# Kernel optimization log

Hardware: AMD Instinct MI355X
Metric: run time of the kernel (lower is better)

## Reference

```python
import jax, jax.numpy as jnp
import numpy as np

B, L, V, E, H, T = 32, 512, 100000, 300, 256, 4  # H = hidden_dim//2 per direction


def setup_inputs() -> dict:
    key = jax.random.key(0)
    ks = jax.random.split(key, 16)
    word_ids = jax.random.randint(ks[0], (B, L), 0, V, dtype=jnp.int32)
    mask = jnp.ones((B, L), dtype=jnp.int32)
    label_ids = jax.random.randint(ks[1], (B, L), 0, T, dtype=jnp.int32)
    emb = jax.random.uniform(ks[2], (V, E), minval=-0.25, maxval=0.25, dtype=jnp.float32)
    emb = emb.at[0].set(0.0)  # padding_idx=0
    w = lambda k, s: jax.random.normal(k, s, dtype=jnp.float32) * 0.05
    return {
        "word_ids": word_ids, "mask": mask, "label_ids": label_ids,
        "emb": emb,
        "Wih_f": w(ks[3], (4 * H, E)), "Whh_f": w(ks[4], (4 * H, H)), "b_f": jnp.zeros((4 * H,), jnp.float32),
        "Wih_b": w(ks[5], (4 * H, E)), "Whh_b": w(ks[6], (4 * H, H)), "b_b": jnp.zeros((4 * H,), jnp.float32),
        "W_out": w(ks[7], (T, 2 * H)), "b_out": jnp.zeros((T,), jnp.float32),
        "transitions": w(ks[8], (T, T)), "start_trans": w(ks[9], (T,)), "end_trans": w(ks[10], (T,)),
    }


def _lstm_dir(x, Wih, Whh, b):
    # x: [B, L, E] -> hs: [B, L, H]; PyTorch gate order i, f, g, o
    xg = jnp.einsum('ble,ge->blg', x, Wih) + b  # [B, L, 4H]
    h0 = jnp.zeros((x.shape[0], Whh.shape[1]), x.dtype)

    def step(carry, g):
        h, c = carry
        gates = g + h @ Whh.T
        i, f, gg, o = jnp.split(gates, 4, axis=-1)
        c = jax.nn.sigmoid(f) * c + jax.nn.sigmoid(i) * jnp.tanh(gg)
        h = jax.nn.sigmoid(o) * jnp.tanh(c)
        return (h, c), h

    _, hs = jax.lax.scan(step, (h0, h0), jnp.swapaxes(xg, 0, 1))
    return jnp.swapaxes(hs, 0, 1)


def _emissions(word_ids, emb, Wih_f, Whh_f, b_f, Wih_b, Whh_b, b_b, W_out, b_out):
    x = emb[word_ids]                                   # [B, L, E]
    h_fwd = _lstm_dir(x, Wih_f, Whh_f, b_f)
    h_bwd = _lstm_dir(x[:, ::-1], Wih_b, Whh_b, b_b)[:, ::-1]
    h = jnp.concatenate([h_fwd, h_bwd], axis=-1)        # [B, L, 2H]
    return h @ W_out.T + b_out                          # [B, L, T]


def _viterbi_decode(emissions, mask, transitions, start_trans, end_trans):
    m = mask.astype(bool)
    score0 = start_trans + emissions[:, 0]              # [B, T]

    def step(score, inp):
        emit_t, mask_t = inp                            # [B,T], [B]
        cand = score[:, :, None] + transitions[None] + emit_t[:, None, :]  # [B, T_from, T_to]
        idx = jnp.argmax(cand, axis=1).astype(jnp.int32)
        new = jnp.max(cand, axis=1)
        return jnp.where(mask_t[:, None], new, score), idx

    score, history = jax.lax.scan(
        step, score0,
        (jnp.swapaxes(emissions[:, 1:], 0, 1), jnp.swapaxes(m[:, 1:], 0, 1)))
    score = score + end_trans
    last_tag = jnp.argmax(score, axis=-1).astype(jnp.int32)  # [B]

    def back(tag, inp):
        idx_t, mask_t = inp
        prev = jnp.take_along_axis(idx_t, tag[:, None], axis=1)[:, 0]
        tag = jnp.where(mask_t, prev, tag)
        return tag, tag

    _, tags_rev = jax.lax.scan(back, last_tag,
                               (history, jnp.swapaxes(m[:, 1:], 0, 1)), reverse=True)
    tags = jnp.concatenate([jnp.swapaxes(tags_rev, 0, 1), last_tag[:, None]], axis=1)  # [B, L]
    return tags * mask.astype(jnp.int32)  # zero out padding like torch y_pred init


def reference(word_ids, mask, label_ids, emb, Wih_f, Whh_f, b_f, Wih_b, Whh_b, b_b,
              W_out, b_out, transitions, start_trans, end_trans):
    emissions = _emissions(word_ids, emb, Wih_f, Whh_f, b_f, Wih_b, Whh_b, b_b, W_out, b_out)
    return _viterbi_decode(emissions, mask, transitions, start_trans, end_trans)
```

## Files before the change

kernel.cpp:

```cpp
#include <hip/hip_runtime.h>
#include <math.h>

#define B_   32
#define L_   512
#define E_   300
#define H_   256
#define T_   4
#define NTOK 16384
#define XGLD 2048
#define SENT 2.0f

typedef float f32x4 __attribute__((ext_vector_type(4)));
typedef float f32x2 __attribute__((ext_vector_type(2)));

__device__ __forceinline__ float fsigmoid_(float x) { return 1.0f / (1.0f + __expf(-x)); }
__device__ __forceinline__ float ftanh_(float x) {
  return 1.0f - 2.0f / (__expf(2.0f * x) + 1.0f);
}

__device__ __forceinline__ void llc_store_f32(float* p, float v) {
  asm volatile("global_store_dword %0, %1, off sc0 sc1" :: "v"(p), "v"(v) : "memory");
}
__device__ __forceinline__ void llc_store_f32x4(float* p, f32x4 v) {
  asm volatile("global_store_dwordx4 %0, %1, off sc0 sc1" :: "v"(p), "v"(v) : "memory");
}
__device__ __forceinline__ f32x4 llc_load_f32x4(const float* p) {
  f32x4 r;
  asm volatile("global_load_dwordx4 %0, %1, off sc0 sc1" : "=&v"(r) : "v"(p) : "memory");
  return r;
}

#define XBM 128
#define XBN 128
#define XBK 20
__global__ __launch_bounds__(256) void xproj_kernel(
    const int*   __restrict__ wid,
    const float* __restrict__ emb,
    const float* __restrict__ wih_f,
    const float* __restrict__ wih_b,
    const float* __restrict__ b_f,
    const float* __restrict__ b_b,
    float* __restrict__ xg,
    float*       h_all,
    int          n4)
{
  __shared__ float Ast[XBK][XBM];
  __shared__ float Bst[XBK][XBN];
  __shared__ int   wid_s[XBM];

  const int tid = threadIdx.x;
  const int m0 = blockIdx.y * XBM;
  const int n0 = blockIdx.x * XBN;
  const int d  = n0 >> 10;
  const float* wih  = d ? wih_b : wih_f;
  const float* bias = d ? b_b  : b_f;
  const int g0 = n0 & 1023;

  if (tid < XBM) wid_s[tid] = wid[m0 + tid];
  __syncthreads();

  const int srow = tid & 127;
  const int half = tid >> 7;
  const float* sbase = half ? (wih + (size_t)(g0 + srow) * E_)
                            : (emb + (size_t)wid_s[srow] * E_);
  float* sdst = half ? &Bst[0][0] : &Ast[0][0];

  f32x4 pre[5];
#pragma unroll
  for (int qd = 0; qd < 5; ++qd) pre[qd] = *(const f32x4*)(sbase + qd * 4);

  const int tx = tid & 15, ty = tid >> 4;
  float acc[8][8] = {};

  for (int k0 = 0; k0 < 300; k0 += XBK) {
#pragma unroll
    for (int qd = 0; qd < 5; ++qd)
#pragma unroll
      for (int e = 0; e < 4; ++e)
        sdst[(qd * 4 + e) * XBM + srow] = pre[qd][e];
    if (k0 + XBK < 300) {
      const float* p = sbase + k0 + XBK;
#pragma unroll
      for (int qd = 0; qd < 5; ++qd) pre[qd] = *(const f32x4*)(p + qd * 4);
    }
    __syncthreads();

#pragma unroll
    for (int k = 0; k < XBK; ++k) {
      float av[8], bv[8];
      *(f32x4*)&av[0] = *(const f32x4*)&Ast[k][ty * 8];
      *(f32x4*)&av[4] = *(const f32x4*)&Ast[k][ty * 8 + 4];
      *(f32x4*)&bv[0] = *(const f32x4*)&Bst[k][tx * 8];
      *(f32x4*)&bv[4] = *(const f32x4*)&Bst[k][tx * 8 + 4];
#pragma unroll
      for (int i = 0; i < 8; ++i)
#pragma unroll
        for (int j = 0; j < 8; ++j)
          acc[i][j] += av[i] * bv[j];
    }
    __syncthreads();
  }

#pragma unroll
  for (int i = 0; i < 8; ++i) {
    const int r = m0 + ty * 8 + i;
    float* op = xg + (size_t)r * XGLD + n0 + tx * 8;
#pragma unroll
    for (int j = 0; j < 8; ++j)
      op[j] = acc[i][j] + bias[g0 + tx * 8 + j];
  }

  {
    const int blin = blockIdx.y * 16 + blockIdx.x;
    f32x4 sv = {SENT, SENT, SENT, SENT};
    for (int i = blin * 256 + tid; i < n4; i += 2048 * 256)
      llc_store_f32x4(h_all + (size_t)i * 4, sv);
  }
}

__global__ __launch_bounds__(512, 2) void lstm_kernel(
    const float* __restrict__ xg,
    const float* __restrict__ whh_f,
    const float* __restrict__ whh_b,
    float*       h_all)
{
  const int bid = blockIdx.x;
  const int d   = bid >> 7;
  const int q   = (bid >> 4) & 7;
  const int sl  = bid & 15;
  const int tid = threadIdx.x;
  const int kp  = tid >> 6;
  const int lane = tid & 63;
  const int bl_loc = lane >> 5;
  const int rg  = lane & 31;
  const float* __restrict__ whh = d ? whh_b : whh_f;

  __shared__ float h_lds[4 * 260];
  __shared__ float part_lds[2 * 8 * 2 * 72];

  f32x4 wreg[2][8];
#pragma unroll
  for (int r = 0; r < 2; ++r) {
    const int row_l = rg * 2 + r;
    const int u  = row_l >> 2;
    const int gt = row_l & 3;
    const int grow = gt * 256 + sl * 16 + u;
    const float* rp = whh + (size_t)grow * H_ + kp * 32;
#pragma unroll
    for (int qq = 0; qq < 8; ++qq) wreg[r][qq] = *(const f32x4*)(rp + qq * 4);
  }

  for (int idx = tid; idx < 4 * 260; idx += 512) h_lds[idx] = 0.f;
  __syncthreads();

  float* hgrp = h_all + (size_t)(d * 8 + q) * (L_ * 1024);

  const int r_u  = (tid & 31) >> 1;
  const int r_bl = (tid < 32) ? (tid & 1) : (2 + (tid & 1));
  float c = 0.f;
  const float* xbase = xg + ((size_t)(q * 4 + r_bl) * L_) * XGLD + d * 1024 + sl * 16 + r_u;
  float x0 = 0.f, x1 = 0.f, x2 = 0.f, x3 = 0.f;
  if (tid < 64) {
    const int t0 = d ? (L_ - 1) : 0;
    const float* xp = xbase + (size_t)t0 * XGLD;
    x0 = xp[0]; x1 = xp[256]; x2 = xp[512]; x3 = xp[768];
  }

#define GEMM_PHASE(PH, BLBASE)                                                \
  do {                                                                        \
    const int blg = (BLBASE) + bl_loc;                                        \
    const float* hb = &h_lds[blg * 260 + kp * 32];                            \
    float a0 = 0.f, a1 = 0.f;                                                 \
    _Pragma("unroll")                                                         \
    for (int i = 0; i < 8; ++i) {                                             \
      f32x4 hv = *(const f32x4*)(hb + i * 4);                                 \
      a0 += wreg[0][i].x * hv.x + wreg[0][i].y * hv.y                         \
          + wreg[0][i].z * hv.z + wreg[0][i].w * hv.w;                        \
      a1 += wreg[1][i].x * hv.x + wreg[1][i].y * hv.y                         \
          + wreg[1][i].z * hv.z + wreg[1][i].w * hv.w;                        \
    }                                                                         \
    f32x2 pv = {a0, a1};                                                      \
    *(f32x2*)&part_lds[(PH) * 1152 + kp * 144 + bl_loc * 72 + rg * 2] = pv;   \
  } while (0)

#define REDUCE_PUBLISH(PH, TT, TN)                                            \
  do {                                                                        \
    f32x4 g = {x0, x1, x2, x3};                                               \
    _Pragma("unroll")                                                         \
    for (int k2 = 0; k2 < 8; ++k2)                                            \
      g += *(const f32x4*)&part_lds[(PH) * 1152 + k2 * 144                    \
                                    + (tid & 1) * 72 + r_u * 4];              \
    float gi = fsigmoid_(g.x);                                                \
    float gf = fsigmoid_(g.y);                                                \
    float gg = ftanh_(g.z);                                                   \
    float go = fsigmoid_(g.w);                                                \
    c = gf * c + gi * gg;                                                     \
    float h = go * ftanh_(c);                                                 \
    llc_store_f32(&hgrp[(size_t)(TT) * 1024 + r_bl * 256 + sl * 16 + r_u], h);\
    if ((TN) >= 0) {                                                          \
      const float* xp = xbase + (size_t)(TN) * XGLD;                          \
      x0 = xp[0]; x1 = xp[256]; x2 = xp[512]; x3 = xp[768];                   \
    }                                                                         \
  } while (0)

#define SPIN_LOAD(BLBASE, TT)                                                 \
  do {                                                                        \
    const int i = tid - 64;                                                   \
    const int blg = (BLBASE) + (i >> 6);                                      \
    const int j4 = (i & 63) * 4;                                              \
    const float* p0 = hgrp + (size_t)(TT) * 1024 + blg * 256 + j4;            \
    f32x4 v0;                                                                 \
    bool bad;                                                                 \
    do {                                                                      \
      v0 = llc_load_f32x4(p0);                                                \
      asm volatile("s_waitcnt vmcnt(0)" ::: "memory");                        \
      __builtin_amdgcn_sched_barrier(0);                                      \
      bad = (v0.x == SENT) | (v0.y == SENT) | (v0.z == SENT) | (v0.w == SENT);\
    } while (bad);                                                            \
    *(f32x4*)&h_lds[blg * 260 + j4] = v0;                                     \
  } while (0)

  for (int s = 0; s < L_; ++s) {
    const int t  = d ? (L_ - 1 - s) : s;
    const int tp = d ? (t + 1) : (t - 1);
    const int tn = (s < L_ - 1) ? (d ? (t - 1) : (t + 1)) : -1;

    GEMM_PHASE(0, 0);
    __syncthreads();

    if (tid < 32) {
      REDUCE_PUBLISH(0, t, tn);
    } else if (s > 0 && tid >= 64 && tid < 192) {
      SPIN_LOAD(2, tp);
    }
    __syncthreads();

    GEMM_PHASE(1, 2);
    __syncthreads();

    if (tid >= 32 && tid < 64) {
      REDUCE_PUBLISH(1, t, tn);
    } else if (s < L_ - 1 && tid >= 64 && tid < 192) {
      SPIN_LOAD(0, t);
    }
    __syncthreads();
  }

#undef GEMM_PHASE
#undef REDUCE_PUBLISH
#undef SPIN_LOAD
}

__global__ __launch_bounds__(256) void emis_kernel(
    const float* __restrict__ h_all,
    const float* __restrict__ wout,
    const float* __restrict__ bout,
    float* __restrict__ em)
{
  __shared__ float hf_l[1024];
  __shared__ float hb_l[1024];
  __shared__ float wsl[2048];

  const int t  = blockIdx.x >> 3;
  const int q  = blockIdx.x & 7;
  const int tid = threadIdx.x;
  const float* hfp = h_all + ((size_t)(0 + q) * L_ + t) * 1024;
  const float* hbp = h_all + ((size_t)(8 + q) * L_ + t) * 1024;

  if (tid < 256) {
    *(f32x4*)&hf_l[tid * 4] = *(const f32x4*)&hfp[tid * 4];
    *(f32x4*)&hb_l[tid * 4] = *(const f32x4*)&hbp[tid * 4];
  }
  for (int i = tid; i < 2048; i += 256) wsl[i] = wout[i];
  __syncthreads();

  const int bl = tid >> 6, lane = tid & 63;
  float s0 = 0.f, s1 = 0.f, s2 = 0.f, s3 = 0.f;
#pragma unroll
  for (int i = 0; i < 4; ++i) {
    const int j = i * 64 + lane;
    const float hfv = hf_l[bl * 256 + j], hbv = hb_l[bl * 256 + j];
    s0 += hfv * wsl[0 * 512 + j] + hbv * wsl[0 * 512 + 256 + j];
    s1 += hfv * wsl[1 * 512 + j] + hbv * wsl[1 * 512 + 256 + j];
    s2 += hfv * wsl[2 * 512 + j] + hbv * wsl[2 * 512 + 256 + j];
    s3 += hfv * wsl[3 * 512 + j] + hbv * wsl[3 * 512 + 256 + j];
  }
#pragma unroll
  for (int m = 1; m < 64; m <<= 1) {
    s0 += __shfl_xor(s0, m, 64);
    s1 += __shfl_xor(s1, m, 64);
    s2 += __shfl_xor(s2, m, 64);
    s3 += __shfl_xor(s3, m, 64);
  }
  if (lane == 0) {
    float* ep = em + ((size_t)(q * 4 + bl) * L_ + t) * 4;
    ep[0] = s0 + bout[0]; ep[1] = s1 + bout[1];
    ep[2] = s2 + bout[2]; ep[3] = s3 + bout[3];
  }
}

__global__ __launch_bounds__(64) void viterbi_kernel(
    const float* __restrict__ em,
    const float* __restrict__ trans,
    const float* __restrict__ strans,
    const float* __restrict__ etrans,
    const int*   __restrict__ mask,
    int* __restrict__ out)
{
  __shared__ float em_l[512 * 4];
  __shared__ int   msk_l[512];
  __shared__ int   hist_l[512 * 4];
  __shared__ int   tags_l[512];

  const int b = blockIdx.x;
  const int tid = threadIdx.x;
  const float* ep = em + (size_t)b * L_ * 4;

  for (int i = tid; i < 512; i += 64) {
    *(f32x4*)&em_l[i * 4] = *(const f32x4*)&ep[i * 4];
    msk_l[i] = mask[b * L_ + i];
  }
  __syncthreads();

  if (tid == 0) {
    float tr[4][4];
#pragma unroll
    for (int i = 0; i < 4; ++i)
#pragma unroll
      for (int jj = 0; jj < 4; ++jj) tr[i][jj] = trans[i * 4 + jj];

    float sc[4];
#pragma unroll
    for (int tag = 0; tag < 4; ++tag) sc[tag] = strans[tag] + em_l[tag];

    for (int t = 1; t < L_; ++t) {
      float ns[4];
#pragma unroll
      for (int to = 0; to < 4; ++to) {
        float best = sc[0] + tr[0][to];
        int bf = 0;
#pragma unroll
        for (int fr = 1; fr < 4; ++fr) {
          float v = sc[fr] + tr[fr][to];
          if (v > best) { best = v; bf = fr; }
        }
        ns[to] = best + em_l[t * 4 + to];
        hist_l[t * 4 + to] = bf;
      }
      const int mt = msk_l[t];
#pragma unroll
      for (int to = 0; to < 4; ++to) sc[to] = mt ? ns[to] : sc[to];
    }

#pragma unroll
    for (int tag = 0; tag < 4; ++tag) sc[tag] += etrans[tag];
    int cur = 0;
    float best = sc[0];
#pragma unroll
    for (int i = 1; i < 4; ++i)
      if (sc[i] > best) { best = sc[i]; cur = i; }

    tags_l[L_ - 1] = msk_l[L_ - 1] ? cur : 0;
    for (int t = L_ - 1; t >= 1; --t) {
      if (msk_l[t]) cur = hist_l[t * 4 + cur];
      tags_l[t - 1] = msk_l[t - 1] ? cur : 0;
    }
  }
  __syncthreads();
  for (int i = tid; i < 512; i += 64) out[b * L_ + i] = tags_l[i];
}

extern "C" void kernel_launch(void* const* d_in, const int* in_sizes, int n_in,
                              void* d_out, int out_size, void* d_ws, size_t ws_size,
                              hipStream_t stream) {
  const int*   word_ids = (const int*)d_in[0];
  const int*   mask     = (const int*)d_in[1];
  const float* emb   = (const float*)d_in[3];
  const float* Wih_f = (const float*)d_in[4];
  const float* Whh_f = (const float*)d_in[5];
  const float* b_f   = (const float*)d_in[6];
  const float* Wih_b = (const float*)d_in[7];
  const float* Whh_b = (const float*)d_in[8];
  const float* b_b   = (const float*)d_in[9];
  const float* W_out = (const float*)d_in[10];
  const float* b_out = (const float*)d_in[11];
  const float* trans = (const float*)d_in[12];
  const float* strans = (const float*)d_in[13];
  const float* etrans = (const float*)d_in[14];
  int* out = (int*)d_out;

  float* xg    = (float*)d_ws;
  float* h_all = xg + (size_t)NTOK * XGLD;
  float* em    = h_all + (size_t)16 * L_ * 1024;

  const int n4 = 16 * L_ * 1024 / 4;
  xproj_kernel<<<dim3(16, 128), 256, 0, stream>>>(word_ids, emb, Wih_f, Wih_b,
                                                  b_f, b_b, xg, h_all, n4);
  lstm_kernel<<<256, 512, 0, stream>>>(xg, Whh_f, Whh_b, h_all);
  emis_kernel<<<4096, 256, 0, stream>>>(h_all, W_out, b_out, em);
  viterbi_kernel<<<32, 64, 0, stream>>>(em, trans, strans, etrans, mask, out);
}
```

Measured before the change: 1.049 ms.

## Split LSTM block into GEMM and reduce/spin warps, cut barriers per step

The recurrent LSTM block is restructured into warp specialisation. Threads 0-255 hold all four gate rows per unit in registers and do the h·Whh products. Threads 256-319 do the reduction and publish, and threads 320-447 spin-load neighbour h from global memory. The phase-1 GEMM now overlaps the phase-0 reduction and the phase-0 GEMM overlaps the spin load, so each timestep needs three barriers instead of four. The cost is doubled register use for the weights in GEMM threads and half the threads doing the dot products.

```diff
diff --git a/kernel.cpp b/kernel.cpp
--- a/kernel.cpp
+++ b/kernel.cpp
@@ -129,25 +129,23 @@
   const int q   = (bid >> 4) & 7;
   const int sl  = bid & 15;
   const int tid = threadIdx.x;
-  const int kp  = tid >> 6;
-  const int lane = tid & 63;
-  const int bl_loc = lane >> 5;
-  const int rg  = lane & 31;
   const float* __restrict__ whh = d ? whh_b : whh_f;
 
   __shared__ float h_lds[4 * 260];
-  __shared__ float part_lds[2 * 8 * 2 * 72];
-
-  f32x4 wreg[2][8];
-#pragma unroll
-  for (int r = 0; r < 2; ++r) {
-    const int row_l = rg * 2 + r;
-    const int u  = row_l >> 2;
-    const int gt = row_l & 3;
-    const int grow = gt * 256 + sl * 16 + u;
-    const float* rp = whh + (size_t)grow * H_ + kp * 32;
-#pragma unroll
-    for (int qq = 0; qq < 8; ++qq) wreg[r][qq] = *(const f32x4*)(rp + qq * 4);
+  __shared__ f32x4 part_lds[2 * 256];
+
+  const int kp   = (tid >> 5) & 7;
+  const int bl_g = (tid >> 4) & 1;
+  const int u_g  = tid & 15;
+  f32x4 wreg[4][8];
+  if (tid < 256) {
+#pragma unroll
+    for (int gt = 0; gt < 4; ++gt) {
+      const int grow = gt * 256 + sl * 16 + u_g;
+      const float* rp = whh + (size_t)grow * H_ + kp * 32;
+#pragma unroll
+      for (int qq = 0; qq < 8; ++qq) wreg[gt][qq] = *(const f32x4*)(rp + qq * 4);
+    }
   }
 
   for (int idx = tid; idx < 4 * 260; idx += 512) h_lds[idx] = 0.f;
@@ -155,12 +153,14 @@
 
   float* hgrp = h_all + (size_t)(d * 8 + q) * (L_ * 1024);
 
-  const int r_u  = (tid & 31) >> 1;
-  const int r_bl = (tid < 32) ? (tid & 1) : (2 + (tid & 1));
+  const int rlane   = tid - 256;
+  const int r_u     = (rlane & 31) >> 1;
+  const int r_bl_lo = rlane & 1;
+  const int r_bl    = ((rlane >> 5) & 1) * 2 + r_bl_lo;
   float c = 0.f;
   const float* xbase = xg + ((size_t)(q * 4 + r_bl) * L_) * XGLD + d * 1024 + sl * 16 + r_u;
   float x0 = 0.f, x1 = 0.f, x2 = 0.f, x3 = 0.f;
-  if (tid < 64) {
+  if (tid >= 256 && tid < 320) {
     const int t0 = d ? (L_ - 1) : 0;
     const float* xp = xbase + (size_t)t0 * XGLD;
     x0 = xp[0]; x1 = xp[256]; x2 = xp[512]; x3 = xp[768];
@@ -168,19 +168,22 @@
 
 #define GEMM_PHASE(PH, BLBASE)                                                \
   do {                                                                        \
-    const int blg = (BLBASE) + bl_loc;                                        \
+    const int blg = (BLBASE) + bl_g;                                          \
     const float* hb = &h_lds[blg * 260 + kp * 32];                            \
-    float a0 = 0.f, a1 = 0.f;                                                 \
+    f32x4 a = {0.f, 0.f, 0.f, 0.f};                                           \
     _Pragma("unroll")                                                         \
     for (int i = 0; i < 8; ++i) {                                             \
       f32x4 hv = *(const f32x4*)(hb + i * 4);                                 \
-      a0 += wreg[0][i].x * hv.x + wreg[0][i].y * hv.y                         \
-          + wreg[0][i].z * hv.z + wreg[0][i].w * hv.w;                        \
-      a1 += wreg[1][i].x * hv.x + wreg[1][i].y * hv.y                         \
-          + wreg[1][i].z * hv.z + wreg[1][i].w * hv.w;                        \
+      a.x += wreg[0][i].x * hv.x + wreg[0][i].y * hv.y                        \
+           + wreg[0][i].z * hv.z + wreg[0][i].w * hv.w;                       \
+      a.y += wreg[1][i].x * hv.x + wreg[1][i].y * hv.y                        \
+           + wreg[1][i].z * hv.z + wreg[1][i].w * hv.w;                       \
+      a.z += wreg[2][i].x * hv.x + wreg[2][i].y * hv.y                        \
+           + wreg[2][i].z * hv.z + wreg[2][i].w * hv.w;                       \
+      a.w += wreg[3][i].x * hv.x + wreg[3][i].y * hv.y                        \
+           + wreg[3][i].z * hv.z + wreg[3][i].w * hv.w;                       \
     }                                                                         \
-    f32x2 pv = {a0, a1};                                                      \
-    *(f32x2*)&part_lds[(PH) * 1152 + kp * 144 + bl_loc * 72 + rg * 2] = pv;   \
+    part_lds[(PH) * 256 + (kp * 2 + bl_g) * 16 + u_g] = a;                    \
   } while (0)
 
 #define REDUCE_PUBLISH(PH, TT, TN)                                            \
@@ -188,8 +191,7 @@
     f32x4 g = {x0, x1, x2, x3};                                               \
     _Pragma("unroll")                                                         \
     for (int k2 = 0; k2 < 8; ++k2)                                            \
-      g += *(const f32x4*)&part_lds[(PH) * 1152 + k2 * 144                    \
-                                    + (tid & 1) * 72 + r_u * 4];              \
+      g += part_lds[(PH) * 256 + (k2 * 2 + r_bl_lo) * 16 + r_u];              \
     float gi = fsigmoid_(g.x);                                                \
     float gf = fsigmoid_(g.y);                                                \
     float gg = ftanh_(g.z);                                                   \
@@ -205,7 +207,7 @@
 
 #define SPIN_LOAD(BLBASE, TT)                                                 \
   do {                                                                        \
-    const int i = tid - 64;                                                   \
+    const int i = tid - 320;                                                  \
     const int blg = (BLBASE) + (i >> 6);                                      \
     const int j4 = (i & 63) * 4;                                              \
     const float* p0 = hgrp + (size_t)(TT) * 1024 + blg * 256 + j4;            \
@@ -225,22 +227,23 @@
     const int tp = d ? (t + 1) : (t - 1);
     const int tn = (s < L_ - 1) ? (d ? (t - 1) : (t + 1)) : -1;
 
-    GEMM_PHASE(0, 0);
+    if (tid < 256) {
+      GEMM_PHASE(0, 0);
+    } else if (s > 0 && tid >= 320 && tid < 448) {
+      SPIN_LOAD(2, tp);
+    }
     __syncthreads();
 
-    if (tid < 32) {
+    if (tid < 256) {
+      GEMM_PHASE(1, 2);
+    } else if (tid >= 256 && tid < 288) {
       REDUCE_PUBLISH(0, t, tn);
-    } else if (s > 0 && tid >= 64 && tid < 192) {
-      SPIN_LOAD(2, tp);
     }
     __syncthreads();
 
-    GEMM_PHASE(1, 2);
-    __syncthreads();
-
-    if (tid >= 32 && tid < 64) {
+    if (tid >= 288 && tid < 320) {
       REDUCE_PUBLISH(1, t, tn);
-    } else if (s < L_ - 1 && tid >= 64 && tid < 192) {
+    } else if (s < L_ - 1 && tid >= 320 && tid < 448) {
       SPIN_LOAD(0, t);
     }
     __syncthreads();
```

New measurement: 1.329 ms. 26.7% more time.

## Fuse emission projection into Viterbi kernel, keeping emissions in shared memory

Applied to the files above, without the earlier changes.

Merges the emission projection kernel and the Viterbi decode kernel into one kernel with 32 blocks of 512 threads. Each block computes the emissions for its own sequence directly into shared memory and then decodes them. This removes one kernel launch and the global write and read of the emissions buffer. In exchange, the projection now runs on only 32 blocks instead of 4096, so less of the GPU is used for that phase.

```diff
diff --git a/kernel.cpp b/kernel.cpp
--- a/kernel.cpp
+++ b/kernel.cpp
@@ -251,56 +251,10 @@
 #undef SPIN_LOAD
 }
 
-__global__ __launch_bounds__(256) void emis_kernel(
+__global__ __launch_bounds__(512) void emvit_kernel(
     const float* __restrict__ h_all,
     const float* __restrict__ wout,
     const float* __restrict__ bout,
-    float* __restrict__ em)
-{
-  __shared__ float hf_l[1024];
-  __shared__ float hb_l[1024];
-  __shared__ float wsl[2048];
-
-  const int t  = blockIdx.x >> 3;
-  const int q  = blockIdx.x & 7;
-  const int tid = threadIdx.x;
-  const float* hfp = h_all + ((size_t)(0 + q) * L_ + t) * 1024;
-  const float* hbp = h_all + ((size_t)(8 + q) * L_ + t) * 1024;
-
-  if (tid < 256) {
-    *(f32x4*)&hf_l[tid * 4] = *(const f32x4*)&hfp[tid * 4];
-    *(f32x4*)&hb_l[tid * 4] = *(const f32x4*)&hbp[tid * 4];
-  }
-  for (int i = tid; i < 2048; i += 256) wsl[i] = wout[i];
-  __syncthreads();
-
-  const int bl = tid >> 6, lane = tid & 63;
-  float s0 = 0.f, s1 = 0.f, s2 = 0.f, s3 = 0.f;
-#pragma unroll
-  for (int i = 0; i < 4; ++i) {
-    const int j = i * 64 + lane;
-    const float hfv = hf_l[bl * 256 + j], hbv = hb_l[bl * 256 + j];
-    s0 += hfv * wsl[0 * 512 + j] + hbv * wsl[0 * 512 + 256 + j];
-    s1 += hfv * wsl[1 * 512 + j] + hbv * wsl[1 * 512 + 256 + j];
-    s2 += hfv * wsl[2 * 512 + j] + hbv * wsl[2 * 512 + 256 + j];
-    s3 += hfv * wsl[3 * 512 + j] + hbv * wsl[3 * 512 + 256 + j];
-  }
-#pragma unroll
-  for (int m = 1; m < 64; m <<= 1) {
-    s0 += __shfl_xor(s0, m, 64);
-    s1 += __shfl_xor(s1, m, 64);
-    s2 += __shfl_xor(s2, m, 64);
-    s3 += __shfl_xor(s3, m, 64);
-  }
-  if (lane == 0) {
-    float* ep = em + ((size_t)(q * 4 + bl) * L_ + t) * 4;
-    ep[0] = s0 + bout[0]; ep[1] = s1 + bout[1];
-    ep[2] = s2 + bout[2]; ep[3] = s3 + bout[3];
-  }
-}
-
-__global__ __launch_bounds__(64) void viterbi_kernel(
-    const float* __restrict__ em,
     const float* __restrict__ trans,
     const float* __restrict__ strans,
     const float* __restrict__ etrans,
@@ -308,17 +262,49 @@
     int* __restrict__ out)
 {
   __shared__ float em_l[512 * 4];
+  __shared__ float wsl[2048];
   __shared__ int   msk_l[512];
   __shared__ int   hist_l[512 * 4];
   __shared__ int   tags_l[512];
 
   const int b = blockIdx.x;
+  const int q = b >> 2, blq = b & 3;
   const int tid = threadIdx.x;
-  const float* ep = em + (size_t)b * L_ * 4;
-
-  for (int i = tid; i < 512; i += 64) {
-    *(f32x4*)&em_l[i * 4] = *(const f32x4*)&ep[i * 4];
-    msk_l[i] = mask[b * L_ + i];
+  const float* hfp = h_all + (size_t)(0 + q) * (L_ * 1024) + blq * 256;
+  const float* hbp = h_all + (size_t)(8 + q) * (L_ * 1024) + blq * 256;
+
+  for (int i = tid; i < 2048; i += 512) wsl[i] = wout[i];
+  if (tid < 512) msk_l[tid] = mask[b * L_ + tid];
+  __syncthreads();
+
+  const int tw = tid >> 6, lane = tid & 63;
+  const float bo0 = bout[0], bo1 = bout[1], bo2 = bout[2], bo3 = bout[3];
+  for (int tt = tw; tt < L_; tt += 8) {
+    const float* hf = hfp + (size_t)tt * 1024;
+    const float* hb = hbp + (size_t)tt * 1024;
+    float s0 = 0.f, s1 = 0.f, s2 = 0.f, s3 = 0.f;
+#pragma unroll
+    for (int i = 0; i < 4; ++i) {
+      const int j = i * 64 + lane;
+      const float hfv = hf[j], hbv = hb[j];
+      s0 += hfv * wsl[j]        + hbv * wsl[256 + j];
+      s1 += hfv * wsl[512 + j]  + hbv * wsl[768 + j];
+      s2 += hfv * wsl[1024 + j] + hbv * wsl[1280 + j];
+      s3 += hfv * wsl[1536 + j] + hbv * wsl[1792 + j];
+    }
+#pragma unroll
+    for (int m = 1; m < 64; m <<= 1) {
+      s0 += __shfl_xor(s0, m, 64);
+      s1 += __shfl_xor(s1, m, 64);
+      s2 += __shfl_xor(s2, m, 64);
+      s3 += __shfl_xor(s3, m, 64);
+    }
+    if (lane == 0) {
+      em_l[tt * 4 + 0] = s0 + bo0;
+      em_l[tt * 4 + 1] = s1 + bo1;
+      em_l[tt * 4 + 2] = s2 + bo2;
+      em_l[tt * 4 + 3] = s3 + bo3;
+    }
   }
   __syncthreads();
 
@@ -367,7 +353,7 @@
     }
   }
   __syncthreads();
-  for (int i = tid; i < 512; i += 64) out[b * L_ + i] = tags_l[i];
+  if (tid < 512) out[b * L_ + tid] = tags_l[tid];
 }
 
 extern "C" void kernel_launch(void* const* d_in, const int* in_sizes, int n_in,
@@ -391,12 +377,11 @@
 
   float* xg    = (float*)d_ws;
   float* h_all = xg + (size_t)NTOK * XGLD;
-  float* em    = h_all + (size_t)16 * L_ * 1024;
 
   const int n4 = 16 * L_ * 1024 / 4;
   xproj_kernel<<<dim3(16, 128), 256, 0, stream>>>(word_ids, emb, Wih_f, Wih_b,
                                                   b_f, b_b, xg, h_all, n4);
   lstm_kernel<<<256, 512, 0, stream>>>(xg, Whh_f, Whh_b, h_all);
-  emis_kernel<<<4096, 256, 0, stream>>>(h_all, W_out, b_out, em);
-  viterbi_kernel<<<32, 64, 0, stream>>>(em, trans, strans, etrans, mask, out);
-}
+  emvit_kernel<<<32, 512, 0, stream>>>(h_all, W_out, b_out, trans, strans,
+                                       etrans, mask, out);
+}
```

Result: slower. 1.099 ms (+4.8%).
